# Performance work log

Measured on AMD Instinct MI355X. Metric: run time of the kernel, lower is better.

## Reference

```python
import jax, jax.numpy as jnp
import numpy as np
from jax import lax

COCO_80_TO_91 = [1,2,3,4,5,6,7,8,9,10,11,13,14,15,16,17,18,19,20,21,22,23,24,25,27,28,31,32,33,34,35,36,37,38,39,40,41,42,43,44,46,47,48,49,50,51,52,53,54,55,56,57,58,59,60,61,62,63,64,65,67,70,72,73,74,75,76,77,78,79,80,81,82,84,85,86,87,88,89,90]

CONF = 0.25      # self.confidence
IOU_THR = 0.7    # ultralytics NMS default
TOPK = 1000      # candidate cap before NMS
MAX_DET = 300    # ultralytics max_det default
MAX_WH = 7680.0  # per-class offset trick
IMG_SZ = 640.0   # yolov8 letterboxed input size


def setup_inputs() -> dict:
    key = jax.random.key(0)
    preds = jax.random.uniform(key, (32, 84, 8400), dtype=jnp.float32)
    return {"preds": preds}


def _nms_single(boxes, scores):
    """Greedy NMS on score-descending boxes [K,4] (class-offset xyxy). Returns keep mask [K]."""
    K = boxes.shape[0]
    area = (boxes[:, 2] - boxes[:, 0]) * (boxes[:, 3] - boxes[:, 1])  # [K]
    lt = jnp.maximum(boxes[:, None, :2], boxes[None, :, :2])          # [K,K,2]
    rb = jnp.minimum(boxes[:, None, 2:], boxes[None, :, 2:])
    wh = jnp.clip(rb - lt, 0.0)
    inter = wh[..., 0] * wh[..., 1]
    iou = inter / (area[:, None] + area[None, :] - inter + 1e-7)       # [K,K]
    idx = jnp.arange(K)
    sup = (iou > IOU_THR) & (idx[None, :] > idx[:, None])              # i suppresses later j

    def body(i, keep):
        return jnp.where(keep[i], keep & ~sup[i], keep)

    return lax.fori_loop(0, K, body, jnp.ones((K,), dtype=bool))


def reference(preds):
    # preds: [B, 84, N] -> [B, N, 84]
    p = jnp.transpose(preds, (0, 2, 1))
    box_xywh = p[..., :4] * IMG_SZ           # xywh in pixels on 640x640 canvas
    cls = p[..., 4:]                          # [B, N, 80]
    scores = jnp.max(cls, axis=-1)            # best-class confidence
    labels = jnp.argmax(cls, axis=-1)         # 0..79
    xy, wh = box_xywh[..., :2], box_xywh[..., 2:]
    xyxy = jnp.concatenate([xy - wh * 0.5, xy + wh * 0.5], axis=-1)  # decode

    # confidence filter + top-K candidate selection (score-descending)
    s_masked = jnp.where(scores > CONF, scores, -1.0)
    top_s, top_i = lax.top_k(s_masked, TOPK)                          # [B,TOPK]
    top_b = jnp.take_along_axis(xyxy, top_i[..., None], axis=1)      # [B,TOPK,4]
    top_l = jnp.take_along_axis(labels, top_i, axis=1)               # [B,TOPK]

    # per-class NMS via class offset
    off_b = top_b + (top_l.astype(top_b.dtype) * MAX_WH)[..., None]
    keep = jax.vmap(_nms_single)(off_b, top_s) & (top_s > CONF)

    # select final max_det detections, zero-pad invalid slots
    fin_s = jnp.where(keep, top_s, -1.0)
    out_s, out_i = lax.top_k(fin_s, MAX_DET)                          # [B,MAX_DET]
    out_b = jnp.take_along_axis(top_b, out_i[..., None], axis=1)
    out_l = jnp.take_along_axis(top_l, out_i, axis=1)
    valid = out_s > CONF
    boxes = jnp.where(valid[..., None], out_b, 0.0)
    scores_out = jnp.where(valid, out_s, 0.0)
    mapped = jnp.asarray(COCO_80_TO_91, dtype=jnp.int64)[out_l]       # COCO 80 -> 91 ids
    labels_out = jnp.where(valid, mapped, 0)
    return boxes, scores_out, labels_out
```

## Files before the change

### kernel.cpp

```cpp
#include <hip/hip_runtime.h>
#include <stdint.h>

typedef unsigned long long u64;
typedef unsigned int u32;

#define BATCH 32
#define NCH 84
#define NA 8400
#define NCLS 80
#define TOPK 1000
#define MAXDET 300
#define CONF 0.25f
#define IOU_T 0.7f
#define MAX_WH 7680.0f
#define IMG_SZ 640.0f
#define NT 1024
#define KPT 9
#define NCOPY 8
#define HPAD 260

__device__ __constant__ float coco_map_f[NCLS] = {
    1,2,3,4,5,6,7,8,9,10,11,13,14,15,16,17,18,19,20,21,22,23,24,25,27,28,
    31,32,33,34,35,36,37,38,39,40,41,42,43,44,46,47,48,49,50,51,52,53,54,
    55,56,57,58,59,60,61,62,63,64,65,67,70,72,73,74,75,76,77,78,79,80,81,
    82,84,85,86,87,88,89,90};

__device__ inline u64 shflx64(u64 v, int m) {
    int lo = __shfl_xor((int)(u32)(v & 0xFFFFFFFFull), m, 64);
    int hi = __shfl_xor((int)(u32)(v >> 32), m, 64);
    return ((u64)(u32)hi << 32) | (u32)lo;
}

__global__ __launch_bounds__(256)
void decode_kernel(const float* __restrict__ preds,
                   u64* __restrict__ keys,
                   float4* __restrict__ boxes) {
    const int b = blockIdx.y;
    const int a = blockIdx.x * 256 + threadIdx.x;
    const bool live = (a < NA);
    const int ac = live ? a : (NA - 1);
    const float* p = preds + (size_t)b * NCH * NA + ac;

    float bx = p[0];
    float by = p[(size_t)1 * NA];
    float bw = p[(size_t)2 * NA];
    float bh = p[(size_t)3 * NA];

    const float* pc = p + (size_t)4 * NA;
    float best = -1.0f;
    int bl = 0;
#pragma unroll 16
    for (int r = 0; r < NCLS; ++r) {
        float v = pc[(size_t)r * NA];
        bl = (v > best) ? r : bl;
        best = fmaxf(v, best);
    }

    if (live) {
        float fx = bx * IMG_SZ, fy = by * IMG_SZ;
        float fw = bw * IMG_SZ, fh = bh * IMG_SZ;
        float hw = fw * 0.5f, hh = fh * 0.5f;
        boxes[(size_t)b * NA + a] = make_float4(fx - hw, fy - hh, fx + hw, fy + hh);
        float s = (best > CONF) ? best : -1.0f;
        u32 fb = __float_as_uint(s);
        u32 u = (fb & 0x80000000u) ? ~fb : (fb | 0x80000000u);
        keys[(size_t)b * NA + a] =
            ((u64)u << 21) | ((u64)(16383 - a) << 7) | (u64)bl;
    }
}

__global__ __launch_bounds__(NT, 4)
void select_sort_kernel(const u64* __restrict__ keys,
                        const float4* __restrict__ boxes,
                        u64* __restrict__ sortedk,
                        float4* __restrict__ gbox,
                        float4* __restrict__ goffb,
                        float* __restrict__ garea,
                        unsigned short* __restrict__ grank,
                        int* __restrict__ gccnt) {
    const int b = blockIdx.x;
    const int t = threadIdx.x;
    const int lane = t & 63, wid = t >> 6;

    __shared__ union {
        struct {
            u64 sk[2][NT];
            int hist[NCOPY * HPAD];
        } a;
        struct {
            u64 cmask2[NCLS][16];
        } bb;
    } u_s;
    __shared__ int selB, selK, hselS, cnt_s;
    __shared__ int wsum[16], woff[16];

    u64 kreg[KPT];
    const u64* kb = keys + (size_t)b * NA;
#pragma unroll
    for (int j = 0; j < KPT; ++j) {
        int i = t + j * NT;
        kreg[j] = (i < NA) ? kb[i] : 0ull;
    }

    u64 P = 0ull;
    int kk = TOPK;
    int nsel = 0;
    bool done = false;
    bool did16 = false;

    {
        int dg[KPT];
        int mymax = -1;
#pragma unroll
        for (int j = 0; j < KPT; ++j) {
            dg[j] = (kreg[j] != 0ull) ? (int)((kreg[j] >> 37) & 0xFFFF) : -1;
            mymax = max(mymax, dg[j]);
        }
#pragma unroll
        for (int off = 32; off; off >>= 1)
            mymax = max(mymax, __shfl_down(mymax, off, 64));
        if (lane == 0) wsum[wid] = mymax;
        __syncthreads();
        int maxd = wsum[0];
#pragma unroll
        for (int q = 1; q < 16; ++q) maxd = max(maxd, wsum[q]);
        int myc = 0;
#pragma unroll
        for (int j = 0; j < KPT; ++j) myc += (dg[j] == maxd) ? 1 : 0;
#pragma unroll
        for (int off = 32; off; off >>= 1) myc += __shfl_down(myc, off, 64);
        if (lane == 0) woff[wid] = myc;
        __syncthreads();
        int cm = 0;
#pragma unroll
        for (int q = 0; q < 16; ++q) cm += woff[q];
        if (cm >= kk) {
            P = ((u64)maxd) << 37;
            nsel = cm;
            did16 = true;
            done = (nsel <= NT);
        }
    }

    if (!done) {
        const int dstart = did16 ? 1 : 3;
        for (int d = dstart; d >= 0; --d) {
            const int sh = 21 + 8 * d;
            const u64 hmask = (~0ull) << (sh + 8);
            int dig[KPT];
            int mymax = -1;
#pragma unroll
            for (int j = 0; j < KPT; ++j) {
                bool act = (((kreg[j] ^ P) & hmask) == 0ull) && (kreg[j] != 0ull);
                dig[j] = act ? (int)((kreg[j] >> sh) & 255) : -1;
                mymax = max(mymax, dig[j]);
            }
#pragma unroll
            for (int off = 32; off; off >>= 1)
                mymax = max(mymax, __shfl_down(mymax, off, 64));
            if (lane == 0) wsum[wid] = mymax;
            __syncthreads();
            int maxb = wsum[0];
#pragma unroll
            for (int q = 1; q < 16; ++q) maxb = max(maxb, wsum[q]);
            int myc = 0;
#pragma unroll
            for (int j = 0; j < KPT; ++j) myc += (dig[j] == maxb) ? 1 : 0;
#pragma unroll
            for (int off = 32; off; off >>= 1) myc += __shfl_down(myc, off, 64);
            if (lane == 0) woff[wid] = myc;
            __syncthreads();
            int cm = 0;
#pragma unroll
            for (int q = 0; q < 16; ++q) cm += woff[q];
            if (cm >= kk) {
                P |= ((u64)maxb) << sh;
                nsel = TOPK - kk + cm;
                if (nsel <= NT) break;
                continue;
            }
            for (int i = t; i < NCOPY * HPAD; i += NT) u_s.a.hist[i] = 0;
            __syncthreads();
            int* myh = u_s.a.hist + (wid & (NCOPY - 1)) * HPAD;
#pragma unroll
            for (int j = 0; j < KPT; ++j)
                if (dig[j] >= 0) atomicAdd(&myh[dig[j]], 1);
            __syncthreads();
            if (t < 64) {
                int h0 = 0, h1 = 0, h2 = 0, h3 = 0;
                for (int c = 0; c < NCOPY; ++c) {
                    const int* hp = u_s.a.hist + c * HPAD + 4 * t;
                    h0 += hp[0]; h1 += hp[1]; h2 += hp[2]; h3 += hp[3];
                }
                int s = h0 + h1 + h2 + h3;
                int S = s;
                #pragma unroll
                for (int off = 1; off < 64; off <<= 1) {
                    int o = __shfl_down(S, off, 64);
                    if (t + off < 64) S += o;
                }
                int Snext = S - s;
                int c3 = Snext + h3, c2 = c3 + h2, c1 = c2 + h1, c0 = c1 + h0;
                int cand = -1, above = 0;
                if (c0 >= kk) {
                    if      (c3 >= kk) { cand = 4 * t + 3; above = Snext; }
                    else if (c2 >= kk) { cand = 4 * t + 2; above = c3; }
                    else if (c1 >= kk) { cand = 4 * t + 1; above = c2; }
                    else               { cand = 4 * t;     above = c1; }
                }
                int pc = (cand < 0) ? 0 : (((cand + 1) << 16) | (kk - above));
                #pragma unroll
                for (int off = 32; off; off >>= 1)
                    pc = max(pc, __shfl_down(pc, off, 64));
                pc = __shfl(pc, 0, 64);
                int B = (pc >> 16) - 1;
                if (t == (B >> 2)) {
                    int m4 = B & 3;
                    selB = B;
                    selK = pc & 0xFFFF;
                    hselS = (m4 == 0) ? h0 : (m4 == 1) ? h1 : (m4 == 2) ? h2 : h3;
                }
            }
            __syncthreads();
            P |= ((u64)selB) << sh;
            kk = selK;
            nsel = TOPK - kk + hselS;
            if (nsel <= NT) break;
        }
    }

    __syncthreads();
    if (t == 0) cnt_s = 0;
    __syncthreads();
#pragma unroll
    for (int j = 0; j < KPT; ++j) {
        bool p = (kreg[j] >= P);
        u64 m = __ballot(p);
        int base = 0;
        if (lane == 0) base = atomicAdd(&cnt_s, (int)__popcll(m));
        base = __shfl(base, 0, 64);
        if (p) {
            int pos = base + (int)__popcll(m & ((1ull << lane) - 1ull));
            if (pos < NT) u_s.a.sk[0][pos] = kreg[j];
        }
    }
    if (t < NT - nsel) u_s.a.sk[0][nsel + t] = 0ull;
    __syncthreads();

    u64 myk = u_s.a.sk[0][t];
    int buf = 1;
    for (int size = 2; size <= NT; size <<= 1) {
        bool up = ((t & size) == 0);
        for (int stride = size >> 1; stride; stride >>= 1) {
            u64 pk;
            if (stride >= 64) {
                u_s.a.sk[buf][t] = myk;
                __syncthreads();
                pk = u_s.a.sk[buf][t ^ stride];
                buf ^= 1;
            } else {
                pk = shflx64(myk, stride);
            }
            bool tlow = ((t & stride) == 0);
            u64 mn = (myk < pk) ? myk : pk;
            u64 mx = (myk < pk) ? pk : myk;
            myk = up ? (tlow ? mx : mn) : (tlow ? mn : mx);
        }
    }
    sortedk[(size_t)b * NT + t] = myk;

    __syncthreads();
    for (int i = t; i < NCLS * 16; i += NT) ((u64*)u_s.bb.cmask2)[i] = 0ull;
    __syncthreads();

    int my_L = 0;
    float4 bx = make_float4(0.f, 0.f, 0.f, 0.f);
    if (t < TOPK) {
        int my_a = 16383 - (int)((myk >> 7) & 16383ull);
        my_L = (int)(myk & 127ull);
        bx = boxes[(size_t)b * NA + my_a];
        atomicOr(&u_s.bb.cmask2[my_L][t >> 6], 1ull << (t & 63));
    }
    __syncthreads();
    if (t < TOPK) {
        int w = t >> 6;
        int r = __popcll(u_s.bb.cmask2[my_L][w] & ((1ull << (t & 63)) - 1ull));
        for (int q = 0; q < w; ++q) r += __popcll(u_s.bb.cmask2[my_L][q]);
        gbox[(size_t)b * NT + t] = bx;
        if (r < 64) {
            float off = (float)my_L * MAX_WH;
            float ox0 = bx.x + off, oy0 = bx.y + off;
            float ox1 = bx.z + off, oy1 = bx.w + off;
            size_t ci = ((size_t)b * NCLS + my_L) * 64 + r;
            goffb[ci] = make_float4(ox0, oy0, ox1, oy1);
            garea[ci] = (ox1 - ox0) * (oy1 - oy0);
            grank[ci] = (unsigned short)t;
        }
    }
    if (t < NCLS) {
        int s = 0;
#pragma unroll
        for (int q = 0; q < 16; ++q) s += __popcll(u_s.bb.cmask2[t][q]);
        gccnt[(size_t)b * NCLS + t] = s;
    }
}

__global__ __launch_bounds__(64)
void nms_kernel(const float4* __restrict__ goffb,
                const float* __restrict__ garea,
                const unsigned short* __restrict__ grank,
                const int* __restrict__ gccnt,
                const u64* __restrict__ sortedk,
                const float4* __restrict__ gbox,
                unsigned char* __restrict__ keepg) {
    const int c = blockIdx.x;
    const int b = blockIdx.y;
    const int lane = threadIdx.x;
    const int n = gccnt[(size_t)b * NCLS + c];
    if (n == 0) return;

    if (n <= 64) {
        size_t ci = ((size_t)b * NCLS + c) * 64 + lane;
        float4 bb = make_float4(0.f, 0.f, 0.f, 0.f);
        float ar = 0.f;
        int rk = 0;
        if (lane < n) { bb = goffb[ci]; ar = garea[ci]; rk = grank[ci]; }
        u64 colm = 0ull;
        for (int i = 0; i < n; ++i) {
            float hx0 = __shfl(bb.x, i, 64);
            float hy0 = __shfl(bb.y, i, 64);
            float hx1 = __shfl(bb.z, i, 64);
            float hy1 = __shfl(bb.w, i, 64);
            float ha  = __shfl(ar, i, 64);
            float lx = fmaxf(hx0, bb.x), ly = fmaxf(hy0, bb.y);
            float rx = fminf(hx1, bb.z), ry = fminf(hy1, bb.w);
            float w = fmaxf(rx - lx, 0.0f);
            float h = fmaxf(ry - ly, 0.0f);
            float inter = w * h;
            float denom = ha + ar;
            denom = denom - inter;
            denom = denom + 1e-7f;
            bool s = (lane > i) && (lane < n) && (inter / denom > IOU_T);
            colm |= ((u64)s) << i;
        }
        u64 alive = (n >= 64) ? ~0ull : ((1ull << n) - 1ull);
        for (int i = 0; i < n; ++i) {
            if (!((alive >> i) & 1ull)) continue;
            alive &= ~__ballot((colm >> i) & 1ull);
        }
        if (lane < n) keepg[(size_t)b * NT + rk] = (unsigned char)((alive >> lane) & 1ull);
    } else if (lane == 0) {
        const u64* skb = sortedk + (size_t)b * NT;
        const float4* gb = gbox + (size_t)b * NT;
        const float off = (float)c * MAX_WH;
        u64 aliveW[16];
        for (int q = 0; q < 16; ++q) aliveW[q] = ~0ull;
        for (int i = 0; i < TOPK; ++i) {
            if ((int)(skb[i] & 127ull) != c) continue;
            if (!((aliveW[i >> 6] >> (i & 63)) & 1ull)) continue;
            float4 g = gb[i];
            float ix0 = g.x + off, iy0 = g.y + off;
            float ix1 = g.z + off, iy1 = g.w + off;
            float ai = (ix1 - ix0) * (iy1 - iy0);
            for (int jj = i + 1; jj < TOPK; ++jj) {
                if ((int)(skb[jj] & 127ull) != c) continue;
                if (!((aliveW[jj >> 6] >> (jj & 63)) & 1ull)) continue;
                float4 h = gb[jj];
                float jx0 = h.x + off, jy0 = h.y + off;
                float jx1 = h.z + off, jy1 = h.w + off;
                float aj = (jx1 - jx0) * (jy1 - jy0);
                float lx = fmaxf(ix0, jx0), ly = fmaxf(iy0, jy0);
                float rx = fminf(ix1, jx1), ry = fminf(iy1, jy1);
                float ww = fmaxf(rx - lx, 0.0f);
                float hh = fmaxf(ry - ly, 0.0f);
                float inter = ww * hh;
                float denom = ai + aj;
                denom = denom - inter;
                denom = denom + 1e-7f;
                if (inter / denom > IOU_T) aliveW[jj >> 6] &= ~(1ull << (jj & 63));
            }
        }
        for (int i = 0; i < TOPK; ++i)
            if ((int)(skb[i] & 127ull) == c)
                keepg[(size_t)b * NT + i] = (unsigned char)((aliveW[i >> 6] >> (i & 63)) & 1ull);
    }
}

__global__ __launch_bounds__(NT)
void epilogue_kernel(const u64* __restrict__ sortedk,
                     const unsigned char* __restrict__ keepg,
                     const float4* __restrict__ gbox,
                     float* __restrict__ out) {
    const int b = blockIdx.x;
    const int t = threadIdx.x;
    const int lane = t & 63, wid = t >> 6;
    __shared__ int wsum[16], woff[16], ktot_s;

    u64 myk = sortedk[(size_t)b * NT + t];
    bool valid = false;
    float sj = 0.0f;
    if (t < TOPK) {
        u32 u = (u32)(myk >> 21);
        u32 fb = (u & 0x80000000u) ? (u ^ 0x80000000u) : ~u;
        sj = __uint_as_float(fb);
        valid = keepg[(size_t)b * NT + t] && (sj > CONF);
    }
    u64 m = __ballot(valid);
    if (lane == 0) wsum[wid] = (int)__popcll(m);
    __syncthreads();
    if (wid == 0) {
        int v = (lane < 16) ? wsum[lane] : 0;
        #pragma unroll
        for (int off = 1; off < 16; off <<= 1) {
            int o = __shfl_up(v, off, 64);
            if (lane >= off) v += o;
        }
        if (lane < 16) woff[lane] = v - wsum[lane];
        if (lane == 15) ktot_s = v;
    }
    __syncthreads();
    int ktot = ktot_s;
    int rank = woff[wid] + (int)__popcll(m & ((1ull << lane) - 1ull));

    float* out_boxes = out;
    float* out_scores = out + (size_t)BATCH * MAXDET * 4;
    float* out_labels = out + (size_t)BATCH * MAXDET * 5;
    if (valid && rank < MAXDET) {
        float4 bx = gbox[(size_t)b * NT + t];
        float* ob = out_boxes + ((size_t)b * MAXDET + rank) * 4;
        ob[0] = bx.x; ob[1] = bx.y; ob[2] = bx.z; ob[3] = bx.w;
        out_scores[(size_t)b * MAXDET + rank] = sj;
        out_labels[(size_t)b * MAXDET + rank] = coco_map_f[(int)(myk & 127ull)];
    }
    if (t < MAXDET && t >= ktot) {
        float* ob = out_boxes + ((size_t)b * MAXDET + t) * 4;
        ob[0] = 0.0f; ob[1] = 0.0f; ob[2] = 0.0f; ob[3] = 0.0f;
        out_scores[(size_t)b * MAXDET + t] = 0.0f;
        out_labels[(size_t)b * MAXDET + t] = 0.0f;
    }
}

extern "C" void kernel_launch(void* const* d_in, const int* in_sizes, int n_in,
                              void* d_out, int out_size, void* d_ws, size_t ws_size,
                              hipStream_t stream) {
    const float* preds = (const float*)d_in[0];
    char* ws = (char*)d_ws;
    size_t off = 0;
    auto alloc = [&](size_t bytes) { char* p = ws + off; off += (bytes + 255) & ~(size_t)255; return p; };

    u64* keys            = (u64*)           alloc((size_t)BATCH * NA * 8);
    float4* boxes        = (float4*)        alloc((size_t)BATCH * NA * 16);
    u64* sortedk         = (u64*)           alloc((size_t)BATCH * NT * 8);
    float4* gbox         = (float4*)        alloc((size_t)BATCH * NT * 16);
    float4* goffb        = (float4*)        alloc((size_t)BATCH * NCLS * 64 * 16);
    float* garea         = (float*)         alloc((size_t)BATCH * NCLS * 64 * 4);
    unsigned short* grank= (unsigned short*)alloc((size_t)BATCH * NCLS * 64 * 2);
    int* gccnt           = (int*)           alloc((size_t)BATCH * NCLS * 4);
    unsigned char* keepg = (unsigned char*) alloc((size_t)BATCH * NT);
    float* out = (float*)d_out;

    dim3 dgrid((NA + 255) / 256, BATCH);
    decode_kernel<<<dgrid, 256, 0, stream>>>(preds, keys, boxes);
    select_sort_kernel<<<BATCH, NT, 0, stream>>>(keys, boxes, sortedk, gbox,
                                                 goffb, garea, grank, gccnt);
    dim3 ngrid(NCLS, BATCH);
    nms_kernel<<<ngrid, 64, 0, stream>>>(goffb, garea, grank, gccnt,
                                         sortedk, gbox, keepg);
    epilogue_kernel<<<BATCH, NT, 0, stream>>>(sortedk, keepg, gbox, out);
}
```

Before: 163.2 us.

## Move per-class bucketing from select-sort kernel into NMS kernel blocks

The per-class grouping (class bitmask, rank computation, scatter of offset boxes/areas/ranks into per-class buffers) is removed from the single-block-per-image sort kernel. Instead, each NMS block scans the 1000 sorted keys with ballots to find its own class members and gathers boxes directly from the decoded box array. This shortens the serial tail of the 32-block sort kernel and drops several intermediate global buffers, at the cost of every one of the 80 per-class blocks rereading the 8 KB sorted key list and doing gather loads.

```diff
diff --git a/kernel.cpp b/kernel.cpp
--- a/kernel.cpp
+++ b/kernel.cpp
@@ -71,25 +71,14 @@
 
 __global__ __launch_bounds__(NT, 4)
 void select_sort_kernel(const u64* __restrict__ keys,
-                        const float4* __restrict__ boxes,
-                        u64* __restrict__ sortedk,
-                        float4* __restrict__ gbox,
-                        float4* __restrict__ goffb,
-                        float* __restrict__ garea,
-                        unsigned short* __restrict__ grank,
-                        int* __restrict__ gccnt) {
+                        u64* __restrict__ sortedk) {
     const int b = blockIdx.x;
     const int t = threadIdx.x;
     const int lane = t & 63, wid = t >> 6;
 
-    __shared__ union {
-        struct {
-            u64 sk[2][NT];
-            int hist[NCOPY * HPAD];
-        } a;
-        struct {
-            u64 cmask2[NCLS][16];
-        } bb;
+    __shared__ struct {
+        u64 sk[2][NT];
+        int hist[NCOPY * HPAD];
     } u_s;
     __shared__ int selB, selK, hselS, cnt_s;
     __shared__ int wsum[16], woff[16];
@@ -179,9 +168,9 @@
                 if (nsel <= NT) break;
                 continue;
             }
-            for (int i = t; i < NCOPY * HPAD; i += NT) u_s.a.hist[i] = 0;
+            for (int i = t; i < NCOPY * HPAD; i += NT) u_s.hist[i] = 0;
             __syncthreads();
-            int* myh = u_s.a.hist + (wid & (NCOPY - 1)) * HPAD;
+            int* myh = u_s.hist + (wid & (NCOPY - 1)) * HPAD;
 #pragma unroll
             for (int j = 0; j < KPT; ++j)
                 if (dig[j] >= 0) atomicAdd(&myh[dig[j]], 1);
@@ -189,7 +178,7 @@
             if (t < 64) {
                 int h0 = 0, h1 = 0, h2 = 0, h3 = 0;
                 for (int c = 0; c < NCOPY; ++c) {
-                    const int* hp = u_s.a.hist + c * HPAD + 4 * t;
+                    const int* hp = u_s.hist + c * HPAD + 4 * t;
                     h0 += hp[0]; h1 += hp[1]; h2 += hp[2]; h3 += hp[3];
                 }
                 int s = h0 + h1 + h2 + h3;
@@ -241,22 +230,22 @@
         base = __shfl(base, 0, 64);
         if (p) {
             int pos = base + (int)__popcll(m & ((1ull << lane) - 1ull));
-            if (pos < NT) u_s.a.sk[0][pos] = kreg[j];
-        }
-    }
-    if (t < NT - nsel) u_s.a.sk[0][nsel + t] = 0ull;
-    __syncthreads();
-
-    u64 myk = u_s.a.sk[0][t];
+            if (pos < NT) u_s.sk[0][pos] = kreg[j];
+        }
+    }
+    if (t < NT - nsel) u_s.sk[0][nsel + t] = 0ull;
+    __syncthreads();
+
+    u64 myk = u_s.sk[0][t];
     int buf = 1;
     for (int size = 2; size <= NT; size <<= 1) {
         bool up = ((t & size) == 0);
         for (int stride = size >> 1; stride; stride >>= 1) {
             u64 pk;
             if (stride >= 64) {
-                u_s.a.sk[buf][t] = myk;
+                u_s.sk[buf][t] = myk;
                 __syncthreads();
-                pk = u_s.a.sk[buf][t ^ stride];
+                pk = u_s.sk[buf][t ^ stride];
                 buf ^= 1;
             } else {
                 pk = shflx64(myk, stride);
@@ -268,63 +257,49 @@
         }
     }
     sortedk[(size_t)b * NT + t] = myk;
-
-    __syncthreads();
-    for (int i = t; i < NCLS * 16; i += NT) ((u64*)u_s.bb.cmask2)[i] = 0ull;
-    __syncthreads();
-
-    int my_L = 0;
-    float4 bx = make_float4(0.f, 0.f, 0.f, 0.f);
-    if (t < TOPK) {
-        int my_a = 16383 - (int)((myk >> 7) & 16383ull);
-        my_L = (int)(myk & 127ull);
-        bx = boxes[(size_t)b * NA + my_a];
-        atomicOr(&u_s.bb.cmask2[my_L][t >> 6], 1ull << (t & 63));
-    }
-    __syncthreads();
-    if (t < TOPK) {
-        int w = t >> 6;
-        int r = __popcll(u_s.bb.cmask2[my_L][w] & ((1ull << (t & 63)) - 1ull));
-        for (int q = 0; q < w; ++q) r += __popcll(u_s.bb.cmask2[my_L][q]);
-        gbox[(size_t)b * NT + t] = bx;
-        if (r < 64) {
-            float off = (float)my_L * MAX_WH;
-            float ox0 = bx.x + off, oy0 = bx.y + off;
-            float ox1 = bx.z + off, oy1 = bx.w + off;
-            size_t ci = ((size_t)b * NCLS + my_L) * 64 + r;
-            goffb[ci] = make_float4(ox0, oy0, ox1, oy1);
-            garea[ci] = (ox1 - ox0) * (oy1 - oy0);
-            grank[ci] = (unsigned short)t;
-        }
-    }
-    if (t < NCLS) {
-        int s = 0;
-#pragma unroll
-        for (int q = 0; q < 16; ++q) s += __popcll(u_s.bb.cmask2[t][q]);
-        gccnt[(size_t)b * NCLS + t] = s;
-    }
 }
 
 __global__ __launch_bounds__(64)
-void nms_kernel(const float4* __restrict__ goffb,
-                const float* __restrict__ garea,
-                const unsigned short* __restrict__ grank,
-                const int* __restrict__ gccnt,
-                const u64* __restrict__ sortedk,
-                const float4* __restrict__ gbox,
+void nms_kernel(const u64* __restrict__ sortedk,
+                const float4* __restrict__ boxes,
                 unsigned char* __restrict__ keepg) {
     const int c = blockIdx.x;
     const int b = blockIdx.y;
     const int lane = threadIdx.x;
-    const int n = gccnt[(size_t)b * NCLS + c];
+    const u64* skb = sortedk + (size_t)b * NT;
+
+    __shared__ int idxs[64];
+
+    int total = 0;
+#pragma unroll
+    for (int i = 0; i < 16; ++i) {
+        int pos = i * 64 + lane;
+        u64 k = skb[pos];
+        bool match = (pos < TOPK) && ((int)(k & 127ull) == c);
+        u64 m = __ballot(match);
+        if (match) {
+            int r = total + (int)__popcll(m & ((1ull << lane) - 1ull));
+            if (r < 64) idxs[r] = pos;
+        }
+        total += (int)__popcll(m);
+    }
+    __syncthreads();
+    const int n = total;
     if (n == 0) return;
 
     if (n <= 64) {
-        size_t ci = ((size_t)b * NCLS + c) * 64 + lane;
         float4 bb = make_float4(0.f, 0.f, 0.f, 0.f);
         float ar = 0.f;
         int rk = 0;
-        if (lane < n) { bb = goffb[ci]; ar = garea[ci]; rk = grank[ci]; }
+        if (lane < n) {
+            rk = idxs[lane];
+            u64 k = skb[rk];
+            int anc = 16383 - (int)((k >> 7) & 16383ull);
+            float4 g = boxes[(size_t)b * NA + anc];
+            float off = (float)c * MAX_WH;
+            bb = make_float4(g.x + off, g.y + off, g.z + off, g.w + off);
+            ar = (bb.z - bb.x) * (bb.w - bb.y);
+        }
         u64 colm = 0ull;
         for (int i = 0; i < n; ++i) {
             float hx0 = __shfl(bb.x, i, 64);
@@ -350,22 +325,22 @@
         }
         if (lane < n) keepg[(size_t)b * NT + rk] = (unsigned char)((alive >> lane) & 1ull);
     } else if (lane == 0) {
-        const u64* skb = sortedk + (size_t)b * NT;
-        const float4* gb = gbox + (size_t)b * NT;
         const float off = (float)c * MAX_WH;
         u64 aliveW[16];
         for (int q = 0; q < 16; ++q) aliveW[q] = ~0ull;
         for (int i = 0; i < TOPK; ++i) {
             if ((int)(skb[i] & 127ull) != c) continue;
             if (!((aliveW[i >> 6] >> (i & 63)) & 1ull)) continue;
-            float4 g = gb[i];
+            int anci = 16383 - (int)((skb[i] >> 7) & 16383ull);
+            float4 g = boxes[(size_t)b * NA + anci];
             float ix0 = g.x + off, iy0 = g.y + off;
             float ix1 = g.z + off, iy1 = g.w + off;
             float ai = (ix1 - ix0) * (iy1 - iy0);
             for (int jj = i + 1; jj < TOPK; ++jj) {
                 if ((int)(skb[jj] & 127ull) != c) continue;
                 if (!((aliveW[jj >> 6] >> (jj & 63)) & 1ull)) continue;
-                float4 h = gb[jj];
+                int ancj = 16383 - (int)((skb[jj] >> 7) & 16383ull);
+                float4 h = boxes[(size_t)b * NA + ancj];
                 float jx0 = h.x + off, jy0 = h.y + off;
                 float jx1 = h.z + off, jy1 = h.w + off;
                 float aj = (jx1 - jx0) * (jy1 - jy0);
@@ -389,7 +364,7 @@
 __global__ __launch_bounds__(NT)
 void epilogue_kernel(const u64* __restrict__ sortedk,
                      const unsigned char* __restrict__ keepg,
-                     const float4* __restrict__ gbox,
+                     const float4* __restrict__ boxes,
                      float* __restrict__ out) {
     const int b = blockIdx.x;
     const int t = threadIdx.x;
@@ -426,7 +401,8 @@
     float* out_scores = out + (size_t)BATCH * MAXDET * 4;
     float* out_labels = out + (size_t)BATCH * MAXDET * 5;
     if (valid && rank < MAXDET) {
-        float4 bx = gbox[(size_t)b * NT + t];
+        int anc = 16383 - (int)((myk >> 7) & 16383ull);
+        float4 bx = boxes[(size_t)b * NA + anc];
         float* ob = out_boxes + ((size_t)b * MAXDET + rank) * 4;
         ob[0] = bx.x; ob[1] = bx.y; ob[2] = bx.z; ob[3] = bx.w;
         out_scores[(size_t)b * MAXDET + rank] = sj;
@@ -451,20 +427,13 @@
     u64* keys            = (u64*)           alloc((size_t)BATCH * NA * 8);
     float4* boxes        = (float4*)        alloc((size_t)BATCH * NA * 16);
     u64* sortedk         = (u64*)           alloc((size_t)BATCH * NT * 8);
-    float4* gbox         = (float4*)        alloc((size_t)BATCH * NT * 16);
-    float4* goffb        = (float4*)        alloc((size_t)BATCH * NCLS * 64 * 16);
-    float* garea         = (float*)         alloc((size_t)BATCH * NCLS * 64 * 4);
-    unsigned short* grank= (unsigned short*)alloc((size_t)BATCH * NCLS * 64 * 2);
-    int* gccnt           = (int*)           alloc((size_t)BATCH * NCLS * 4);
     unsigned char* keepg = (unsigned char*) alloc((size_t)BATCH * NT);
     float* out = (float*)d_out;
 
     dim3 dgrid((NA + 255) / 256, BATCH);
     decode_kernel<<<dgrid, 256, 0, stream>>>(preds, keys, boxes);
-    select_sort_kernel<<<BATCH, NT, 0, stream>>>(keys, boxes, sortedk, gbox,
-                                                 goffb, garea, grank, gccnt);
+    select_sort_kernel<<<BATCH, NT, 0, stream>>>(keys, sortedk);
     dim3 ngrid(NCLS, BATCH);
-    nms_kernel<<<ngrid, 64, 0, stream>>>(goffb, garea, grank, gccnt,
-                                         sortedk, gbox, keepg);
-    epilogue_kernel<<<BATCH, NT, 0, stream>>>(sortedk, keepg, gbox, out);
-}
+    nms_kernel<<<ngrid, 64, 0, stream>>>(sortedk, boxes, keepg);
+    epilogue_kernel<<<BATCH, NT, 0, stream>>>(sortedk, keepg, boxes, out);
+}
```

Result: no change. 163.3 us (+0.1%).
